# Optimization experiments

Measured on AMD Instinct MI355X. Metric: run time of the kernel, lower is better.

## Reference

```python
import jax, jax.numpy as jnp
import numpy as np

K = 4
TEMP = 0.5
PAD = 1

def setup_inputs() -> dict:
    key = jax.random.key(0)
    ks = jax.random.split(key, 5)
    B, C, H, W = 32, 256, 64, 64
    O, HID = 256, 65  # int(256*0.25)+1
    x = jax.random.normal(ks[0], (B, C, H, W), dtype=jnp.float32)
    w1 = jax.random.normal(ks[1], (HID, C), dtype=jnp.float32) * 0.05
    w2 = jax.random.normal(ks[2], (K * O, HID), dtype=jnp.float32) * 0.05
    b2 = jnp.zeros((K * O,), dtype=jnp.float32)
    weight = jax.random.normal(ks[3], (K, O, C, 3, 3), dtype=jnp.float32) * 0.05
    return {"x": x, "w1": w1, "w2": w2, "b2": b2, "weight": weight}

def _dyn_conv(x, w1, w2, b2, weight):
    B, C, H, W = x.shape
    Kk, O = weight.shape[0], weight.shape[1]
    # GPM2d attention: global avg pool -> 1x1 conv -> relu -> 1x1 conv -> softmax over K
    pooled = jnp.mean(x, axis=(2, 3))                     # [B, C]
    h = jax.nn.relu(pooled @ w1.T)                        # [B, HID]
    logits = (h @ w2.T + b2).reshape(B, Kk, O)            # [B, K, O]
    attn = jax.nn.softmax(logits / TEMP, axis=1)          # softmax over K experts
    # aggregate per-sample, per-out-channel weights: [B, O, C, k, k]
    agg_w = jnp.einsum('bko,kocij->bocij', attn, weight)
    # per-sample conv (equivalent to groups=batch trick in torch)
    def conv1(xi, wi):
        return jax.lax.conv_general_dilated(
            xi[None], wi, window_strides=(1, 1),
            padding=[(PAD, PAD), (PAD, PAD)],
            dimension_numbers=('NCHW', 'OIHW', 'NCHW'))[0]
    return jax.vmap(conv1)(x, agg_w)                      # [B, O, H, W]

def reference(x, w1, w2, b2, weight):
    return _dyn_conv(x, w1, w2, b2, weight)
```

## Files before the change

kernel.cpp:

```cpp
#include <hip/hip_runtime.h>
#include <stdint.h>

typedef unsigned short ushort_t;
typedef __attribute__((ext_vector_type(8))) short short8;
typedef __attribute__((ext_vector_type(8))) unsigned short ushortx8;
typedef __attribute__((ext_vector_type(4))) float floatx4;

#define B_    32
#define C_    256
#define O_    256
#define HID_  65
#define HW_   4096
#define KDIM  2304
#define XP_H  66
#define XPAD_ELEMS ((size_t)B_ * XP_H * XP_H * C_)
#define WAGG_ELEMS ((size_t)B_ * O_ * KDIM)

static __device__ __forceinline__ unsigned short f2bf(float f) {
  unsigned u = __float_as_uint(f);
  u += 0x7fffu + ((u >> 16) & 1u);
  return (unsigned short)(u >> 16);
}

static __device__ __forceinline__ void gld_lds16(const void* g, void* l) {
  __builtin_amdgcn_global_load_lds((__attribute__((address_space(1))) void*)(g),
                                   (__attribute__((address_space(3))) void*)(l),
                                   16, 0, 0);
}

__global__ void border_kernel(ushort_t* __restrict__ xpad) {
  const int b = blockIdx.x, t = threadIdx.x;
  uint4 z = {0u, 0u, 0u, 0u};
  uint4* base = (uint4*)(xpad + (size_t)b * XP_H * XP_H * C_);
  for (int i = t; i < 2112; i += 256) {
    base[i] = z;
    base[(size_t)65 * 2112 + i] = z;
  }
  for (int i = t; i < 64 * 32; i += 256) {
    const int h = 1 + (i >> 5), s = i & 31;
    base[(size_t)h * 2112 + s] = z;
    base[(size_t)h * 2112 + 65 * 32 + s] = z;
  }
}

__global__ void pad_kernel(const float* __restrict__ x, ushort_t* __restrict__ xpad,
                           float* __restrict__ partial) {
  __shared__ float tileT[64][65];
  __shared__ float pool[4][64];
  const int hwT = blockIdx.x, cT = blockIdx.y, b = blockIdx.z;
  const int t = threadIdx.x;
  const int hw0 = hwT * 64, c0 = cT * 64;
  const float* src = x + ((size_t)(b * C_ + c0)) * HW_ + hw0;

#pragma unroll
  for (int p = 0; p < 4; ++p) {
    const int flat = p * 256 + t;
    const int c = flat >> 4, h4 = (flat & 15) * 4;
    const float4 v = *(const float4*)(src + (size_t)c * HW_ + h4);
    tileT[h4 + 0][c] = v.x;
    tileT[h4 + 1][c] = v.y;
    tileT[h4 + 2][c] = v.z;
    tileT[h4 + 3][c] = v.w;
  }
  __syncthreads();

  {
    const int c = t & 63, qh = t >> 6;
    float s = 0.f;
#pragma unroll
    for (int i = 0; i < 16; ++i) s += tileT[qh * 16 + i][c];
    pool[qh][c] = s;
  }
  __syncthreads();
  if (t < 64) {
    partial[(size_t)hwT * (B_ * C_) + b * C_ + c0 + t] =
        pool[0][t] + pool[1][t] + pool[2][t] + pool[3][t];
  }

#pragma unroll
  for (int p = 0; p < 2; ++p) {
    const int flat = p * 256 + t;
    const int hw = flat >> 3, cg = (flat & 7) * 8;
    ushortx8 v;
#pragma unroll
    for (int j = 0; j < 8; ++j) v[j] = f2bf(tileT[hw][cg + j]);
    const int h = (hw0 + hw) >> 6, w = (hw0 + hw) & 63;
    *(ushortx8*)(xpad + (((size_t)b * XP_H + (h + 1)) * XP_H + (w + 1)) * C_ + c0 + cg) = v;
  }
}

__global__ void attn_kernel(const float* __restrict__ partial,
                            const float* __restrict__ w1,
                            const float* __restrict__ w2,
                            const float* __restrict__ b2,
                            float* __restrict__ attn) {
  __shared__ float sp[C_];
  __shared__ float sh[HID_];
  const int b = blockIdx.x, t = threadIdx.x;
  {
    float s = 0.f;
#pragma unroll
    for (int i = 0; i < 64; ++i) s += partial[(size_t)i * (B_ * C_) + b * C_ + t];
    sp[t] = s * (1.f / 4096.f);
  }
  __syncthreads();
  if (t < HID_) {
    float a = 0.f;
    for (int c = 0; c < C_; ++c) a += sp[c] * w1[t * C_ + c];
    sh[t] = fmaxf(a, 0.f);
  }
  __syncthreads();
  float lg[4];
#pragma unroll
  for (int k = 0; k < 4; ++k) {
    float a = b2[k * O_ + t];
    for (int j = 0; j < HID_; ++j) a += sh[j] * w2[(k * O_ + t) * HID_ + j];
    lg[k] = a * 2.0f;
  }
  float mx = fmaxf(fmaxf(lg[0], lg[1]), fmaxf(lg[2], lg[3]));
  float e0 = expf(lg[0] - mx), e1 = expf(lg[1] - mx);
  float e2 = expf(lg[2] - mx), e3 = expf(lg[3] - mx);
  float inv = 1.f / (e0 + e1 + e2 + e3);
  attn[(b * 4 + 0) * O_ + t] = e0 * inv;
  attn[(b * 4 + 1) * O_ + t] = e1 * inv;
  attn[(b * 4 + 2) * O_ + t] = e2 * inv;
  attn[(b * 4 + 3) * O_ + t] = e3 * inv;
}

__global__ void agg_kernel(const float* __restrict__ attn,
                           const float* __restrict__ wt,
                           ushort_t* __restrict__ wagg) {
  const int o = blockIdx.x;
  const int b0 = blockIdx.y * 4;
  const int t = threadIdx.x;
  float wr[4][9];
#pragma unroll
  for (int k = 0; k < 4; ++k) {
    const float* src = wt + (size_t)(k * O_ + o) * KDIM + t * 9;
#pragma unroll
    for (int n = 0; n < 9; ++n) wr[k][n] = src[n];
  }
#pragma unroll
  for (int bi = 0; bi < 4; ++bi) {
    const int b = b0 + bi;
    const float a0 = attn[(b * 4 + 0) * O_ + o];
    const float a1 = attn[(b * 4 + 1) * O_ + o];
    const float a2 = attn[(b * 4 + 2) * O_ + o];
    const float a3 = attn[(b * 4 + 3) * O_ + o];
    ushort_t* dst = wagg + (size_t)(b * O_ + o) * KDIM;
#pragma unroll
    for (int n = 0; n < 9; ++n) {
      float v = a0 * wr[0][n] + a1 * wr[1][n] + a2 * wr[2][n] + a3 * wr[3][n];
      dst[n * C_ + t] = f2bf(v);
    }
  }
}

__global__ __launch_bounds__(256) void gemm_kernel(const ushort_t* __restrict__ xpad,
                                                   const ushort_t* __restrict__ wagg,
                                                   float* __restrict__ out) {
  __shared__ short lA[128 * 64];
  __shared__ short lB[128 * 64];

  const int hwT = blockIdx.x;
  const int oT  = blockIdx.y;
  const int b   = blockIdx.z;
  const int t    = threadIdx.x;
  const int lane = t & 63;
  const int wv   = t >> 6;

  const int hwBase = hwT << 7;
  const int h0     = hwT << 1;
  const int oBase  = oT << 7;

  const int rS = lane >> 3;
  const int pS = lane & 7;
  size_t aG[4], bG[4];
  int ldsOff[4];
#pragma unroll
  for (int q = 0; q < 4; ++q) {
    const int row = wv * 32 + q * 8 + rS;
    const int lch = pS ^ (row & 7);
    aG[q] = (size_t)(b * O_ + oBase + row) * KDIM + lch * 8;
    const int hl = row >> 6, wl2 = row & 63;
    bG[q] = ((size_t)(b * XP_H + h0 + hl) * XP_H + wl2) * C_ + lch * 8;
    ldsOff[q] = (wv * 32 + q * 8) * 64;
  }

  const int lm   = lane & 15;
  const int quad = lane >> 4;
  const int mW = (wv & 1) << 6;
  const int nW = (wv >> 1) << 6;
  int aOff[2][4], bOff[2][4];
#pragma unroll
  for (int h = 0; h < 2; ++h)
#pragma unroll
    for (int i = 0; i < 4; ++i) {
      const int ps = ((h * 4 + quad) ^ (lm & 7)) * 8;
      aOff[h][i] = (mW + i * 16 + lm) * 64 + ps;
      bOff[h][i] = (nW + i * 16 + lm) * 64 + ps;
    }

  floatx4 acc[4][4] = {};

  for (int tap = 0; tap < 9; ++tap) {
    const int toff = (tap / 3) * XP_H + (tap % 3);
#pragma unroll 1
    for (int c0 = 0; c0 < C_; c0 += 64) {
      const int kk = tap * C_ + c0;
      __syncthreads();
#pragma unroll
      for (int q = 0; q < 4; ++q) {
        gld_lds16(wagg + aG[q] + kk, lA + ldsOff[q]);
        gld_lds16(xpad + bG[q] + (size_t)toff * C_ + c0, lB + ldsOff[q]);
      }
      __builtin_amdgcn_s_waitcnt(0x0f70);
      __syncthreads();

#pragma unroll
      for (int h = 0; h < 2; ++h) {
        short8 af[4], bf[4];
#pragma unroll
        for (int i = 0; i < 4; ++i) af[i] = *(const short8*)(lA + aOff[h][i]);
#pragma unroll
        for (int i = 0; i < 4; ++i) bf[i] = *(const short8*)(lB + bOff[h][i]);
#pragma unroll
        for (int mi = 0; mi < 4; ++mi)
#pragma unroll
          for (int ni = 0; ni < 4; ++ni)
            acc[mi][ni] = __builtin_amdgcn_mfma_f32_16x16x32_bf16(
                af[mi], bf[ni], acc[mi][ni], 0, 0, 0);
      }
    }
  }

  const size_t outBase = (size_t)b * O_ * HW_;
#pragma unroll
  for (int mi = 0; mi < 4; ++mi) {
#pragma unroll
    for (int ni = 0; ni < 4; ++ni) {
      const int hw = hwBase + nW + ni * 16 + lm;
#pragma unroll
      for (int r = 0; r < 4; ++r) {
        const int o = oBase + mW + mi * 16 + quad * 4 + r;
        out[outBase + (size_t)o * HW_ + hw] = acc[mi][ni][r];
      }
    }
  }
}

extern "C" void kernel_launch(void* const* d_in, const int* in_sizes, int n_in,
                              void* d_out, int out_size, void* d_ws, size_t ws_size,
                              hipStream_t stream) {
  const float* x  = (const float*)d_in[0];
  const float* w1 = (const float*)d_in[1];
  const float* w2 = (const float*)d_in[2];
  const float* b2 = (const float*)d_in[3];
  const float* wt = (const float*)d_in[4];
  float* out = (float*)d_out;

  char* ws = (char*)d_ws;
  ushort_t* xpad = (ushort_t*)ws;
  ushort_t* wagg = (ushort_t*)(ws + XPAD_ELEMS * 2);
  float* partial = (float*)(ws + XPAD_ELEMS * 2 + WAGG_ELEMS * 2);
  float* attn    = partial + 64 * B_ * C_;

  border_kernel<<<B_, 256, 0, stream>>>(xpad);
  pad_kernel<<<dim3(64, 4, B_), 256, 0, stream>>>(x, xpad, partial);
  attn_kernel<<<B_, 256, 0, stream>>>(partial, w1, w2, b2, attn);
  agg_kernel<<<dim3(O_, 8), 256, 0, stream>>>(attn, wt, wagg);
  gemm_kernel<<<dim3(32, 2, B_), 256, 0, stream>>>(xpad, wagg, out);
}
```

Before: 445.7 us.

## Remap GEMM blocks so each XCD owns whole batches; fold border zeroing into pad

The GEMM grid is flattened and block ids are remapped so that all blocks of a given batch sample land on the same XCD. Blocks that share a sample's padded input and aggregated weights can then reuse them in that XCD's L2 instead of spreading across all eight. Zeroing of the padding border moves into the pad kernel's cT==0 blocks, which removes one kernel launch. The remap assumes round-robin block dispatch across eight XCDs.

```diff
diff --git a/kernel.cpp b/kernel.cpp
--- a/kernel.cpp
+++ b/kernel.cpp
@@ -28,21 +28,6 @@
                                    16, 0, 0);
 }
 
-__global__ void border_kernel(ushort_t* __restrict__ xpad) {
-  const int b = blockIdx.x, t = threadIdx.x;
-  uint4 z = {0u, 0u, 0u, 0u};
-  uint4* base = (uint4*)(xpad + (size_t)b * XP_H * XP_H * C_);
-  for (int i = t; i < 2112; i += 256) {
-    base[i] = z;
-    base[(size_t)65 * 2112 + i] = z;
-  }
-  for (int i = t; i < 64 * 32; i += 256) {
-    const int h = 1 + (i >> 5), s = i & 31;
-    base[(size_t)h * 2112 + s] = z;
-    base[(size_t)h * 2112 + 65 * 32 + s] = z;
-  }
-}
-
 __global__ void pad_kernel(const float* __restrict__ x, ushort_t* __restrict__ xpad,
                            float* __restrict__ partial) {
   __shared__ float tileT[64][65];
@@ -51,6 +36,25 @@
   const int t = threadIdx.x;
   const int hw0 = hwT * 64, c0 = cT * 64;
   const float* src = x + ((size_t)(b * C_ + c0)) * HW_ + hw0;
+
+  if (cT == 0) {
+    const int tid = hwT * 256 + t;
+    if (tid < 8320) {
+      uint4 z = {0u, 0u, 0u, 0u};
+      uint4* base = (uint4*)(xpad + (size_t)b * XP_H * XP_H * C_);
+      size_t idx;
+      if (tid < 2112) idx = (size_t)tid;
+      else if (tid < 4224) idx = (size_t)65 * 2112 + (tid - 2112);
+      else if (tid < 6272) {
+        const int i = tid - 4224;
+        idx = (size_t)(1 + (i >> 5)) * 2112 + (i & 31);
+      } else {
+        const int i = tid - 6272;
+        idx = (size_t)(1 + (i >> 5)) * 2112 + 65 * 32 + (i & 31);
+      }
+      base[idx] = z;
+    }
+  }
 
 #pragma unroll
   for (int p = 0; p < 4; ++p) {
@@ -162,9 +166,13 @@
   __shared__ short lA[128 * 64];
   __shared__ short lB[128 * 64];
 
-  const int hwT = blockIdx.x;
-  const int oT  = blockIdx.y;
-  const int b   = blockIdx.z;
+  const int bid = blockIdx.x;
+  const int xcd = bid & 7;
+  const int q   = bid >> 3;
+  const int b   = xcd + ((q >> 6) << 3);
+  const int oT  = (q >> 5) & 1;
+  const int hwT = q & 31;
+
   const int t    = threadIdx.x;
   const int lane = t & 63;
   const int wv   = t >> 6;
@@ -178,13 +186,13 @@
   size_t aG[4], bG[4];
   int ldsOff[4];
 #pragma unroll
-  for (int q = 0; q < 4; ++q) {
-    const int row = wv * 32 + q * 8 + rS;
+  for (int qq = 0; qq < 4; ++qq) {
+    const int row = wv * 32 + qq * 8 + rS;
     const int lch = pS ^ (row & 7);
-    aG[q] = (size_t)(b * O_ + oBase + row) * KDIM + lch * 8;
+    aG[qq] = (size_t)(b * O_ + oBase + row) * KDIM + lch * 8;
     const int hl = row >> 6, wl2 = row & 63;
-    bG[q] = ((size_t)(b * XP_H + h0 + hl) * XP_H + wl2) * C_ + lch * 8;
-    ldsOff[q] = (wv * 32 + q * 8) * 64;
+    bG[qq] = ((size_t)(b * XP_H + h0 + hl) * XP_H + wl2) * C_ + lch * 8;
+    ldsOff[qq] = (wv * 32 + qq * 8) * 64;
   }
 
   const int lm   = lane & 15;
@@ -210,9 +218,9 @@
       const int kk = tap * C_ + c0;
       __syncthreads();
 #pragma unroll
-      for (int q = 0; q < 4; ++q) {
-        gld_lds16(wagg + aG[q] + kk, lA + ldsOff[q]);
-        gld_lds16(xpad + bG[q] + (size_t)toff * C_ + c0, lB + ldsOff[q]);
+      for (int qq = 0; qq < 4; ++qq) {
+        gld_lds16(wagg + aG[qq] + kk, lA + ldsOff[qq]);
+        gld_lds16(xpad + bG[qq] + (size_t)toff * C_ + c0, lB + ldsOff[qq]);
       }
       __builtin_amdgcn_s_waitcnt(0x0f70);
       __syncthreads();
@@ -265,9 +273,8 @@
   float* partial = (float*)(ws + XPAD_ELEMS * 2 + WAGG_ELEMS * 2);
   float* attn    = partial + 64 * B_ * C_;
 
-  border_kernel<<<B_, 256, 0, stream>>>(xpad);
   pad_kernel<<<dim3(64, 4, B_), 256, 0, stream>>>(x, xpad, partial);
   attn_kernel<<<B_, 256, 0, stream>>>(partial, w1, w2, b2, attn);
   agg_kernel<<<dim3(O_, 8), 256, 0, stream>>>(attn, wt, wagg);
-  gemm_kernel<<<dim3(32, 2, B_), 256, 0, stream>>>(xpad, wagg, out);
-}
+  gemm_kernel<<<2048, 256, 0, stream>>>(xpad, wagg, out);
+}
```

Measured after the change: 432.9 us. 1.03x faster.
